# Kernel tuning notes

Hardware: AMD Instinct MI355X
Metric: run time of the kernel (lower is better)

Reference implementation:

```python
import jax, jax.numpy as jnp
import numpy as np

NEG_SLOPE = 0.01  # torch nn.LeakyReLU default

B, N, IN_F, OUT_F, HEADS = 4, 2048, 512, 512, 8
D = OUT_F // HEADS  # 64


def setup_inputs() -> dict:
    key = jax.random.key(0)
    ks = jax.random.split(key, 4)
    X = jax.random.normal(ks[0], (B, N, IN_F), dtype=jnp.float32)
    W_v = jax.random.normal(ks[1], (IN_F, D), dtype=jnp.float32) * (IN_F ** -0.5)
    b_v = jnp.zeros((D,), dtype=jnp.float32)
    W_q = jax.random.normal(ks[2], (D, HEADS), dtype=jnp.float32) * (D ** -0.5)
    b_q = jnp.zeros((HEADS,), dtype=jnp.float32)
    W_k = jax.random.normal(ks[3], (D, HEADS), dtype=jnp.float32) * (D ** -0.5)
    b_k = jnp.zeros((HEADS,), dtype=jnp.float32)
    return {"X": X, "W_v": W_v, "b_v": b_v, "W_q": W_q, "b_q": b_q, "W_k": W_k, "b_k": b_k}


def reference(X, W_v, b_v, W_q, b_q, W_k, b_k):
    # V: (B, N, D)
    V = X @ W_v + b_v
    # per-node, per-head scalar scores: (B, N, H) -> (B, H, N)
    Q = jnp.swapaxes(V @ W_q + b_q, 1, 2)
    K = jnp.swapaxes(V @ W_k + b_k, 1, 2)
    # A[b,h,i,j] = leaky_relu(Q[b,h,j] + K[b,h,i])  (broadcast outer-sum)
    A = jax.nn.leaky_relu(Q[:, :, None, :] + K[:, :, :, None], negative_slope=NEG_SLOPE)
    A = jax.nn.softmax(A, axis=-1)  # dropout = identity in eval mode
    # H[b,i,h,f] = sum_j A[b,h,i,j] V[b,j,f]
    H = jnp.einsum('bhij,bjf->bihf', A, V)
    return H.reshape(H.shape[0], H.shape[1], -1)  # (B, N, H*D)
```

## Files before the change

### kernel.cpp

```cpp
#include <hip/hip_runtime.h>

#define BB   4
#define NN   2048
#define INF  512
#define HH   8
#define DD   64
#define BH   (BB*HH)
#define NCK  16
#define CKS  128
#define KSP  2


__global__ __launch_bounds__(256) void k_v(
    const float* __restrict__ X, const float* __restrict__ Wv,
    float* __restrict__ Vpart)
{
  __shared__ float Ws[64][68];
  const int t  = threadIdx.x;
  const int tc = t & 15;
  const int tr = t >> 4;
  const int rg = blockIdx.x >> 1;
  const int kh = blockIdx.x & 1;
  const int r0 = rg * 32;
  const int k0 = kh * 256;
  float acc[2][4] = {{0.f}};

  for (int kc = 0; kc < 256; kc += 64) {
    __syncthreads();
    #pragma unroll
    for (int i = 0; i < 4; i++) {
      const int e4 = t + i * 256;
      const int k  = e4 >> 4;
      const int n4 = (e4 & 15) * 4;
      *(float4*)(&Ws[k][n4]) = *(const float4*)(Wv + (size_t)(k0 + kc + k) * DD + n4);
    }
    __syncthreads();
    const float* xp0 = X + (size_t)(r0 + tr * 2) * INF + k0 + kc;
    const float* xp1 = xp0 + INF;
    #pragma unroll 8
    for (int kk = 0; kk < 64; kk += 4) {
      const float4 xa = *(const float4*)(xp0 + kk);
      const float4 xb = *(const float4*)(xp1 + kk);
      #pragma unroll
      for (int j = 0; j < 4; j++) {
        const float4 w4 = *(const float4*)(&Ws[kk + j][tc * 4]);
        const float xaj = (j == 0) ? xa.x : (j == 1) ? xa.y : (j == 2) ? xa.z : xa.w;
        const float xbj = (j == 0) ? xb.x : (j == 1) ? xb.y : (j == 2) ? xb.z : xb.w;
        acc[0][0] += xaj * w4.x;  acc[0][1] += xaj * w4.y;
        acc[0][2] += xaj * w4.z;  acc[0][3] += xaj * w4.w;
        acc[1][0] += xbj * w4.x;  acc[1][1] += xbj * w4.y;
        acc[1][2] += xbj * w4.z;  acc[1][3] += xbj * w4.w;
      }
    }
  }
  float* vp = Vpart + ((size_t)kh * (BB*NN) + r0 + tr * 2) * DD + tc * 4;
  #pragma unroll
  for (int r = 0; r < 2; r++) {
    float4 o;  o.x = acc[r][0];  o.y = acc[r][1];  o.z = acc[r][2];  o.w = acc[r][3];
    *(float4*)(vp + (size_t)r * DD) = o;
  }
}

__global__ __launch_bounds__(256) void k_vred(
    const float* __restrict__ Vpart, const float* __restrict__ bv,
    const float* __restrict__ Wq, const float* __restrict__ bq,
    const float* __restrict__ Wk, const float* __restrict__ bk,
    float* __restrict__ V, float* __restrict__ qsg, float* __restrict__ ksg,
    unsigned long long* __restrict__ qk64)
{
  __shared__ float Vs[16][DD + 1];
  const int t  = threadIdx.x;
  const size_t e0 = ((size_t)blockIdx.x * 256 + t) * 4;
  const size_t STR = (size_t)BB * NN * DD;
  float4 a = *(const float4*)(Vpart + e0);
  #pragma unroll
  for (int p = 1; p < KSP; p++) {
    const float4 b = *(const float4*)(Vpart + (size_t)p * STR + e0);
    a.x += b.x;  a.y += b.y;  a.z += b.z;  a.w += b.w;
  }
  const float4 bb = *(const float4*)(bv + (e0 & 63));
  a.x += bb.x;  a.y += bb.y;  a.z += bb.z;  a.w += bb.w;
  *(float4*)(V + e0) = a;
  const int lrow = t >> 4;
  const int lcol = (t * 4) & 63;
  Vs[lrow][lcol]   = a.x;  Vs[lrow][lcol+1] = a.y;
  Vs[lrow][lcol+2] = a.z;  Vs[lrow][lcol+3] = a.w;
  __syncthreads();
  const int row = t >> 4;
  const int h   = t & 7;
  const bool isK = (t & 8) != 0;
  const float* W = isK ? Wk : Wq;
  float s = isK ? bk[h] : bq[h];
  #pragma unroll 8
  for (int dd = 0; dd < DD; dd++) s += Vs[row][dd] * W[dd*HH + h];
  const int grow = blockIdx.x * 16 + row;
  const int b = grow >> 11, n = grow & (NN - 1);
  (isK ? ksg : qsg)[(b*HH + h) * NN + n] = s;
  if (!isK) {
    unsigned u = __float_as_uint(s);
    u = (u & 0x80000000u) ? ~u : (u | 0x80000000u);
    qk64[(size_t)(b*HH + h) * NN + n] =
        ((unsigned long long)u << 32) | (unsigned)n;
  }
}

__global__ __launch_bounds__(256) void k_rank(
    const unsigned long long* __restrict__ qk64,
    float* __restrict__ sqs, unsigned short* __restrict__ idxg)
{
  __shared__ __align__(16) unsigned long long keys[NN];
  __shared__ int cnt[4][256];
  const int t  = threadIdx.x;
  const int bh = blockIdx.x >> 3;
  const int jq = t & 63;
  const int kq = t >> 6;
  const unsigned long long* __restrict__ kb = qk64 + (size_t)bh * NN;

  {
    const ulonglong2* __restrict__ g2 = (const ulonglong2*)kb;
    ulonglong2* s2 = (ulonglong2*)keys;
    #pragma unroll
    for (int x = 0; x < 4; x++) s2[t + 256 * x] = g2[t + 256 * x];
  }
  __syncthreads();

  const int jg = ((blockIdx.x & 7) << 8) | (jq << 2);
  const unsigned long long kj0 = keys[jg];
  const unsigned long long kj1 = keys[jg + 1];
  const unsigned long long kj2 = keys[jg + 2];
  const unsigned long long kj3 = keys[jg + 3];

  const ulonglong2* __restrict__ k2 = (const ulonglong2*)(keys + kq * 512);
  int c0 = 0, c1 = 0, c2 = 0, c3 = 0;
  #pragma unroll 8
  for (int l = 0; l < 256; l++) {
    const ulonglong2 kk = k2[l];
    c0 += (kk.x < kj0) + (kk.y < kj0);
    c1 += (kk.x < kj1) + (kk.y < kj1);
    c2 += (kk.x < kj2) + (kk.y < kj2);
    c3 += (kk.x < kj3) + (kk.y < kj3);
  }
  cnt[kq][0 * 64 + jq] = c0;
  cnt[kq][1 * 64 + jq] = c1;
  cnt[kq][2 * 64 + jq] = c2;
  cnt[kq][3 * 64 + jq] = c3;
  __syncthreads();

  if (kq == 0) {
    #pragma unroll
    for (int u = 0; u < 4; u++) {
      const int rank = cnt[0][u * 64 + jq] + cnt[1][u * 64 + jq]
                     + cnt[2][u * 64 + jq] + cnt[3][u * 64 + jq];
      const unsigned long long kj = keys[jg + u];
      const unsigned uo = (unsigned)(kj >> 32);
      const unsigned ur = (uo & 0x80000000u) ? (uo & 0x7fffffffu) : ~uo;
      sqs [bh * NN + rank] = __uint_as_float(ur);
      idxg[bh * NN + rank] = (unsigned short)(jg + u);
    }
  }
}

__global__ __launch_bounds__(256) void k_scan(
    const float* __restrict__ sq, const unsigned short* __restrict__ idxg,
    const float* __restrict__ V,
    float* __restrict__ P1, float* __restrict__ P2,
    float* __restrict__ l1, float* __restrict__ l2,
    float* __restrict__ S1g, float* __restrict__ S2g,
    float* __restrict__ SL1, float* __restrict__ SL2)
{
  __shared__ float vstash[4][32][DD];
  __shared__ float ss1[4][64], ss2[4][64], sl1[4], sl2[4];
  const int t  = threadIdx.x;
  const int bh = blockIdx.x >> 4;
  const int ck = blockIdx.x & 15;
  const int d  = t & 63, g = t >> 6;
  const int r0 = ck*CKS + g*32;
  const float* Vb  = V + (size_t)(bh >> 3) * NN * DD;
  const float* sqb = sq + bh*NN;
  const unsigned short* ib = idxg + bh*NN;
  float a1 = 0.f, a2 = 0.f, s1 = 0.f, s2 = 0.f;
  #pragma unroll 8
  for (int rr = 0; rr < 32; rr++) {
    const int r = r0 + rr;
    const float qv = sqb[r];
    const float e1 = __expf(qv), e2 = __expf(0.01f*qv);
    const float v  = Vb[(size_t)ib[r]*DD + d];
    vstash[g][rr][d] = v;
    a1 += e1*v;  a2 += e2*v;  s1 += e1;  s2 += e2;
  }
  ss1[g][d] = a1;  ss2[g][d] = a2;
  if (d == 0) { sl1[g] = s1;  sl2[g] = s2; }
  __syncthreads();
  float o1 = 0.f, o2 = 0.f, lo1 = 0.f, lo2 = 0.f;
  for (int gg = 0; gg < g; gg++) { o1 += ss1[gg][d]; o2 += ss2[gg][d]; lo1 += sl1[gg]; lo2 += sl2[gg]; }
  if (g == 0) {
    S1g[(bh*NCK + ck)*64 + d] = ss1[0][d]+ss1[1][d]+ss1[2][d]+ss1[3][d];
    S2g[(bh*NCK + ck)*64 + d] = ss2[0][d]+ss2[1][d]+ss2[2][d]+ss2[3][d];
    if (d == 0) {
      SL1[bh*NCK + ck] = sl1[0]+sl1[1]+sl1[2]+sl1[3];
      SL2[bh*NCK + ck] = sl2[0]+sl2[1]+sl2[2]+sl2[3];
    }
  }
  a1 = o1; a2 = o2; s1 = lo1; s2 = lo2;
  float* P1b = P1 + (size_t)bh*NN*DD;
  float* P2b = P2 + (size_t)bh*NN*DD;
  #pragma unroll 8
  for (int rr = 0; rr < 32; rr++) {
    const int r = r0 + rr;
    const float qv = sqb[r];
    const float e1 = __expf(qv), e2 = __expf(0.01f*qv);
    const float v  = vstash[g][rr][d];
    P1b[(size_t)r*DD + d] = a1;
    P2b[(size_t)r*DD + d] = a2;
    if (d == 0) { l1[bh*NN + r] = s1;  l2[bh*NN + r] = s2; }
    a1 += e1*v;  a2 += e2*v;  s1 += e1;  s2 += e2;
  }
}

__global__ __launch_bounds__(256) void k_out(
    const float* __restrict__ sq, const float* __restrict__ ksg,
    const float* __restrict__ P1, const float* __restrict__ P2,
    const float* __restrict__ S1g, const float* __restrict__ S2g,
    const float* __restrict__ SL1, const float* __restrict__ SL2,
    const float* __restrict__ l1, const float* __restrict__ l2,
    float* __restrict__ out)
{
  __shared__ float Of1[NCK + 1][64], Of2[NCK + 1][64];
  __shared__ float Lo1[NCK + 1], Lo2[NCK + 1];
  const int t   = threadIdx.x;
  const int bh  = blockIdx.x >> 7;
  const int loc = blockIdx.x & 127;
  const int w   = t >> 6;
  const int d   = t & 63;
  const int i0  = loc*16 + w*4;
  const int b   = bh >> 3, h = bh & 7;

  if (t < 64) {
    float a = 0.f;
    for (int ck = 0; ck < NCK; ck++) {
      Of1[ck][t] = a;  a += S1g[(bh*NCK + ck)*64 + t];
    }
    Of1[NCK][t] = a;
  } else if (t < 128) {
    const int dd = t - 64;
    float a = 0.f;
    for (int ck = 0; ck < NCK; ck++) {
      Of2[ck][dd] = a;  a += S2g[(bh*NCK + ck)*64 + dd];
    }
    Of2[NCK][dd] = a;
  } else if (t == 128) {
    float a = 0.f;
    for (int ck = 0; ck < NCK; ck++) { Lo1[ck] = a;  a += SL1[bh*NCK + ck]; }
    Lo1[NCK] = a;
  } else if (t == 129) {
    float a = 0.f;
    for (int ck = 0; ck < NCK; ck++) { Lo2[ck] = a;  a += SL2[bh*NCK + ck]; }
    Lo2[NCK] = a;
  }
  __syncthreads();

  const float* s = sq + bh*NN;
  const float probe = s[d*32 + 31];
  const float T1  = Of1[NCK][d];
  const float Lt1 = Lo1[NCK];
  const size_t base = (size_t)bh * NN * DD;

  float kv[4], tt[4];
  int pos[4];
  #pragma unroll
  for (int u = 0; u < 4; u++) { kv[u] = ksg[bh*NN + i0 + u];  tt[u] = -kv[u]; }
  #pragma unroll
  for (int u = 0; u < 4; u++) {
    const unsigned long long m1 = __ballot(probe <= tt[u]);
    const int c1 = __popcll(m1);
    if (c1 == 64) pos[u] = NN;
    else {
      const unsigned long long m2 = __ballot(s[c1*32 + (d & 31)] <= tt[u]);
      pos[u] = c1*32 + (__popcll(m2) >> 1);
    }
  }
  #pragma unroll
  for (int u = 0; u < 4; u++) {
    const float ek  = __expf(kv[u]);
    const float ek2 = __expf(0.01f * kv[u]);
    float p1v, p2v, q1v, q2v;
    if (pos[u] < NN) {
      const int ch = pos[u] >> 7;
      p1v = P1[base + (size_t)pos[u]*DD + d] + Of1[ch][d];
      p2v = P2[base + (size_t)pos[u]*DD + d] + Of2[ch][d];
      q1v = l1[bh*NN + pos[u]] + Lo1[ch];
      q2v = l2[bh*NN + pos[u]] + Lo2[ch];
    } else {
      p1v = T1;   p2v = Of2[NCK][d];
      q1v = Lt1;  q2v = Lo2[NCK];
    }
    const float num = ek * (T1 - p1v)  + ek2 * p2v;
    const float den = ek * (Lt1 - q1v) + ek2 * q2v;
    out[((size_t)(b*NN + i0 + u)) * (HH*DD) + h*DD + d] = num / den;
  }
}

extern "C" void kernel_launch(void* const* d_in, const int* in_sizes, int n_in,
                              void* d_out, int out_size, void* d_ws, size_t ws_size,
                              hipStream_t stream)
{
  (void)in_sizes; (void)n_in; (void)out_size; (void)ws_size;
  const float* X  = (const float*)d_in[0];
  const float* Wv = (const float*)d_in[1];
  const float* bv = (const float*)d_in[2];
  const float* Wq = (const float*)d_in[3];
  const float* bq = (const float*)d_in[4];
  const float* Wk = (const float*)d_in[5];
  const float* bk = (const float*)d_in[6];
  float* out = (float*)d_out;

  float* w = (float*)d_ws;
  float* V     = w;  w += (size_t)BB*NN*DD;
  float* qsg   = w;  w += BH*NN;
  float* ksg   = w;  w += BH*NN;
  float* l1    = w;  w += BH*NN;
  float* l2    = w;  w += BH*NN;
  unsigned short* idxg = (unsigned short*)w;  w += BH*NN/2;
  float* S1g   = w;  w += (size_t)BH*NCK*DD;
  float* S2g   = w;  w += (size_t)BH*NCK*DD;
  float* SL1   = w;  w += BH*NCK;
  float* SL2   = w;  w += BH*NCK;
  float* sqs   = w;  w += BH*NN;
  unsigned long long* qk64 = (unsigned long long*)w;  w += BH*NN*2;
  float* P1    = w;  w += (size_t)BH*NN*DD;
  float* P2    = w;  w += (size_t)BH*NN*DD;

  float* Vpart = P1;

  k_v    <<<512, 256, 0, stream>>>(X, Wv, Vpart);
  k_vred <<<512, 256, 0, stream>>>(Vpart, bv, Wq, bq, Wk, bk, V, qsg, ksg, qk64);
  k_rank <<<BH*8, 256, 0, stream>>>(qk64, sqs, idxg);
  k_scan <<<BH*NCK, 256, 0, stream>>>(sqs, idxg, V, P1, P2, l1, l2, S1g, S2g, SL1, SL2);
  k_out  <<<BH*128, 256, 0, stream>>>(sqs, ksg, P1, P2, S1g, S2g, SL1, SL2, l1, l2, out);
}
```

Baseline: 135.7 us.

## Fuse V projection, split-K reduction and Q/K score computation into one kernel

```diff
diff --git a/kernel.cpp b/kernel.cpp
--- a/kernel.cpp
+++ b/kernel.cpp
@@ -8,100 +8,103 @@
 #define BH   (BB*HH)
 #define NCK  16
 #define CKS  128
-#define KSP  2
-
-
-__global__ __launch_bounds__(256) void k_v(
+
+
+__global__ __launch_bounds__(256) void k_vq(
     const float* __restrict__ X, const float* __restrict__ Wv,
-    float* __restrict__ Vpart)
-{
-  __shared__ float Ws[64][68];
-  const int t  = threadIdx.x;
-  const int tc = t & 15;
-  const int tr = t >> 4;
-  const int rg = blockIdx.x >> 1;
-  const int kh = blockIdx.x & 1;
-  const int r0 = rg * 32;
-  const int k0 = kh * 256;
-  float acc[2][4] = {{0.f}};
-
-  for (int kc = 0; kc < 256; kc += 64) {
-    __syncthreads();
-    #pragma unroll
-    for (int i = 0; i < 4; i++) {
-      const int e4 = t + i * 256;
-      const int k  = e4 >> 4;
-      const int n4 = (e4 & 15) * 4;
-      *(float4*)(&Ws[k][n4]) = *(const float4*)(Wv + (size_t)(k0 + kc + k) * DD + n4);
-    }
-    __syncthreads();
-    const float* xp0 = X + (size_t)(r0 + tr * 2) * INF + k0 + kc;
-    const float* xp1 = xp0 + INF;
-    #pragma unroll 8
-    for (int kk = 0; kk < 64; kk += 4) {
-      const float4 xa = *(const float4*)(xp0 + kk);
-      const float4 xb = *(const float4*)(xp1 + kk);
-      #pragma unroll
-      for (int j = 0; j < 4; j++) {
-        const float4 w4 = *(const float4*)(&Ws[kk + j][tc * 4]);
-        const float xaj = (j == 0) ? xa.x : (j == 1) ? xa.y : (j == 2) ? xa.z : xa.w;
-        const float xbj = (j == 0) ? xb.x : (j == 1) ? xb.y : (j == 2) ? xb.z : xb.w;
-        acc[0][0] += xaj * w4.x;  acc[0][1] += xaj * w4.y;
-        acc[0][2] += xaj * w4.z;  acc[0][3] += xaj * w4.w;
-        acc[1][0] += xbj * w4.x;  acc[1][1] += xbj * w4.y;
-        acc[1][2] += xbj * w4.z;  acc[1][3] += xbj * w4.w;
-      }
-    }
-  }
-  float* vp = Vpart + ((size_t)kh * (BB*NN) + r0 + tr * 2) * DD + tc * 4;
-  #pragma unroll
-  for (int r = 0; r < 2; r++) {
-    float4 o;  o.x = acc[r][0];  o.y = acc[r][1];  o.z = acc[r][2];  o.w = acc[r][3];
-    *(float4*)(vp + (size_t)r * DD) = o;
-  }
-}
-
-__global__ __launch_bounds__(256) void k_vred(
-    const float* __restrict__ Vpart, const float* __restrict__ bv,
+    const float* __restrict__ bv,
     const float* __restrict__ Wq, const float* __restrict__ bq,
     const float* __restrict__ Wk, const float* __restrict__ bk,
     float* __restrict__ V, float* __restrict__ qsg, float* __restrict__ ksg,
     unsigned long long* __restrict__ qk64)
 {
-  __shared__ float Vs[16][DD + 1];
+  __shared__ float Ws[2][64][68];
+  __shared__ float red[128][16];
+  __shared__ float Vs[32][65];
   const int t  = threadIdx.x;
-  const size_t e0 = ((size_t)blockIdx.x * 256 + t) * 4;
-  const size_t STR = (size_t)BB * NN * DD;
-  float4 a = *(const float4*)(Vpart + e0);
+  const int kh = t >> 7;
+  const int u  = t & 127;
+  const int tc = u & 15;
+  const int rg = u >> 4;
+  const int r0 = blockIdx.x * 32;
+  const int k0 = kh * 256;
+  float acc[4][4];
   #pragma unroll
-  for (int p = 1; p < KSP; p++) {
-    const float4 b = *(const float4*)(Vpart + (size_t)p * STR + e0);
-    a.x += b.x;  a.y += b.y;  a.z += b.z;  a.w += b.w;
-  }
-  const float4 bb = *(const float4*)(bv + (e0 & 63));
-  a.x += bb.x;  a.y += bb.y;  a.z += bb.z;  a.w += bb.w;
-  *(float4*)(V + e0) = a;
-  const int lrow = t >> 4;
-  const int lcol = (t * 4) & 63;
-  Vs[lrow][lcol]   = a.x;  Vs[lrow][lcol+1] = a.y;
-  Vs[lrow][lcol+2] = a.z;  Vs[lrow][lcol+3] = a.w;
-  __syncthreads();
-  const int row = t >> 4;
+  for (int r = 0; r < 4; r++)
+    #pragma unroll
+    for (int c = 0; c < 4; c++) acc[r][c] = 0.f;
+
+  for (int kc = 0; kc < 256; kc += 64) {
+    __syncthreads();
+    #pragma unroll
+    for (int i = 0; i < 8; i++) {
+      const int e4 = u + i * 128;
+      const int k  = e4 >> 4;
+      const int n4 = (e4 & 15) * 4;
+      *(float4*)(&Ws[kh][k][n4]) =
+          *(const float4*)(Wv + (size_t)(k0 + kc + k) * DD + n4);
+    }
+    __syncthreads();
+    const float* xp = X + (size_t)(r0 + rg * 4) * INF + k0 + kc;
+    #pragma unroll 4
+    for (int kk = 0; kk < 64; kk += 4) {
+      float4 xr[4];
+      #pragma unroll
+      for (int r = 0; r < 4; r++)
+        xr[r] = *(const float4*)(xp + (size_t)r * INF + kk);
+      #pragma unroll
+      for (int j = 0; j < 4; j++) {
+        const float4 w4 = *(const float4*)(&Ws[kh][kk + j][tc * 4]);
+        #pragma unroll
+        for (int r = 0; r < 4; r++) {
+          const float x = (j == 0) ? xr[r].x : (j == 1) ? xr[r].y
+                        : (j == 2) ? xr[r].z : xr[r].w;
+          acc[r][0] += x * w4.x;  acc[r][1] += x * w4.y;
+          acc[r][2] += x * w4.z;  acc[r][3] += x * w4.w;
+        }
+      }
+    }
+  }
+
+  __syncthreads();
+  if (kh == 1) {
+    #pragma unroll
+    for (int r = 0; r < 4; r++)
+      *(float4*)(&red[u][r * 4]) = *(const float4*)(&acc[r][0]);
+  }
+  __syncthreads();
+  if (kh == 0) {
+    const float4 bb = *(const float4*)(bv + tc * 4);
+    #pragma unroll
+    for (int r = 0; r < 4; r++) {
+      const float4 p = *(const float4*)(&red[u][r * 4]);
+      float4 o;
+      o.x = acc[r][0] + p.x + bb.x;  o.y = acc[r][1] + p.y + bb.y;
+      o.z = acc[r][2] + p.z + bb.z;  o.w = acc[r][3] + p.w + bb.w;
+      *(float4*)(V + (size_t)(r0 + rg * 4 + r) * DD + tc * 4) = o;
+      Vs[rg * 4 + r][tc * 4]     = o.x;  Vs[rg * 4 + r][tc * 4 + 1] = o.y;
+      Vs[rg * 4 + r][tc * 4 + 2] = o.z;  Vs[rg * 4 + r][tc * 4 + 3] = o.w;
+    }
+  }
+  __syncthreads();
+
+  const int row = t >> 3;
   const int h   = t & 7;
-  const bool isK = (t & 8) != 0;
-  const float* W = isK ? Wk : Wq;
-  float s = isK ? bk[h] : bq[h];
+  float sq = bq[h], sk = bk[h];
   #pragma unroll 8
-  for (int dd = 0; dd < DD; dd++) s += Vs[row][dd] * W[dd*HH + h];
-  const int grow = blockIdx.x * 16 + row;
+  for (int dd = 0; dd < DD; dd++) {
+    const float v = Vs[row][dd];
+    sq += v * Wq[dd * HH + h];
+    sk += v * Wk[dd * HH + h];
+  }
+  const int grow = r0 + row;
   const int b = grow >> 11, n = grow & (NN - 1);
-  (isK ? ksg : qsg)[(b*HH + h) * NN + n] = s;
-  if (!isK) {
-    unsigned u = __float_as_uint(s);
-    u = (u & 0x80000000u) ? ~u : (u | 0x80000000u);
-    qk64[(size_t)(b*HH + h) * NN + n] =
-        ((unsigned long long)u << 32) | (unsigned)n;
-  }
+  const int bh = b * HH + h;
+  qsg[bh * NN + n] = sq;
+  ksg[bh * NN + n] = sk;
+  unsigned uo = __float_as_uint(sq);
+  uo = (uo & 0x80000000u) ? ~uo : (uo | 0x80000000u);
+  qk64[(size_t)bh * NN + n] = ((unsigned long long)uo << 32) | (unsigned)n;
 }
 
 __global__ __launch_bounds__(256) void k_rank(
@@ -330,10 +333,7 @@
   float* P1    = w;  w += (size_t)BH*NN*DD;
   float* P2    = w;  w += (size_t)BH*NN*DD;
 
-  float* Vpart = P1;
-
-  k_v    <<<512, 256, 0, stream>>>(X, Wv, Vpart);
-  k_vred <<<512, 256, 0, stream>>>(Vpart, bv, Wq, bq, Wk, bk, V, qsg, ksg, qk64);
+  k_vq   <<<256, 256, 0, stream>>>(X, Wv, bv, Wq, bq, Wk, bk, V, qsg, ksg, qk64);
   k_rank <<<BH*8, 256, 0, stream>>>(qk64, sqs, idxg);
   k_scan <<<BH*NCK, 256, 0, stream>>>(sqs, idxg, V, P1, P2, l1, l2, S1g, S2g, SL1, SL2);
   k_out  <<<BH*128, 256, 0, stream>>>(sqs, ksg, P1, P2, S1g, S2g, SL1, SL2, l1, l2, out);
```

After: 133.7 us. About the same (-1.5%).
